# Kernel tuning notes

Measured on AMD Instinct MI355X. Metric: run time of the kernel, lower is better.

## Reference

```python
import jax, jax.numpy as jnp
import numpy as np

B, N, D, O, H, R = 32, 1024, 1024, 1024, 512, 64
TOPK = 4
MAX_GAIN = 0.1
SCALE = 1.0
LN_EPS = 1e-5


def _dct_basis(dim, num_bases):
    pos = np.arange(dim, dtype=np.float64)[None, :]
    modes = np.arange(num_bases, dtype=np.float64)[:, None]
    basis = np.cos(np.pi / dim * (pos + 0.5) * modes)
    basis[0] = basis[0] / np.sqrt(2.0)
    basis = basis * np.sqrt(2.0 / dim)
    return jnp.asarray(basis, jnp.float32)


def setup_inputs() -> dict:
    key = jax.random.key(0)
    ks = jax.random.split(key, 16)
    s = 0.02
    return {
        'x': jax.random.normal(ks[0], (B, N, D), jnp.float32),
        'context': jax.random.normal(ks[1], (B, H), jnp.float32),
        'input_basis': _dct_basis(D, R),                       # [R, D] (buffer)
        'output_basis': s * jax.random.normal(ks[2], (R, O), jnp.float32),
        'ln_gamma': jnp.ones((D,), jnp.float32),
        'ln_beta': jnp.zeros((D,), jnp.float32),
        'w1': s * jax.random.normal(ks[3], (D, H), jnp.float32),
        'b1': jnp.zeros((H,), jnp.float32),
        'w2': s * jax.random.normal(ks[4], (H, H), jnp.float32),
        'b2': jnp.zeros((H,), jnp.float32),
        'wg': s * jax.random.normal(ks[5], (H, R * R), jnp.float32),
        'bg': jnp.zeros((R * R,), jnp.float32),
        'wl': s * jax.random.normal(ks[6], (H, R * R), jnp.float32),
        'bl': jnp.zeros((R * R,), jnp.float32),
        'wm': s * jax.random.normal(ks[7], (2 * H, R), jnp.float32),
        'bm': 1.5 * jnp.ones((R,), jnp.float32),
        'wgain': s * jax.random.normal(ks[8], (2 * H, R), jnp.float32),
        'bgain': jnp.zeros((R,), jnp.float32),
        'wgate': s * jax.random.normal(ks[9], (2 * H, 1), jnp.float32),
        'bgate': -1.0 * jnp.ones((1,), jnp.float32),
        'wa': s * jax.random.normal(ks[10], (2 * H, 1), jnp.float32),
        'ba': -1.0 * jnp.ones((1,), jnp.float32),
        'wb': s * jax.random.normal(ks[11], (2 * H, 1), jnp.float32),
        'bb': jnp.zeros((1,), jnp.float32),
    }


def _detail_summary(x, topk):
    # x: [B, N, D] with token 0 = CLS; pick topk highest-variance patch tokens
    pt = x[:, 1:]                                   # [B, N-1, D]
    pm = jnp.mean(pt, axis=1, keepdims=True)
    scores = jnp.mean((pt - pm) ** 2, axis=-1)      # [B, N-1]
    _, idx = jax.lax.top_k(scores, topk)            # [B, k]
    gathered = jnp.take_along_axis(pt, idx[:, :, None], axis=1)  # [B, k, D]
    return jnp.mean(gathered, axis=1)               # [B, D]


def _skew(a):
    return 0.5 * (a - jnp.swapaxes(a, -1, -2))


def reference(x, context, input_basis, output_basis, ln_gamma, ln_beta,
              w1, b1, w2, b2, wg, bg, wl, bl, wm, bm,
              wgain, bgain, wgate, bgate, wa, ba, wb, bb):
    b = x.shape[0]
    r = input_basis.shape[0]

    detail = _detail_summary(x, TOPK)               # [B, D]
    mu = jnp.mean(detail, axis=-1, keepdims=True)
    var = jnp.var(detail, axis=-1, keepdims=True)
    h = (detail - mu) * jax.lax.rsqrt(var + LN_EPS) * ln_gamma + ln_beta
    h = jax.nn.gelu(h @ w1 + b1, approximate=False)
    local_context = h @ w2 + b2                     # [B, H]
    fused = jnp.concatenate([context, local_context], axis=-1)  # [B, 2H]

    global_skew = _skew((context @ wg + bg).reshape(b, r, r))
    local_skew = _skew((local_context @ wl + bl).reshape(b, r, r))
    mode_mask = jax.nn.sigmoid(fused @ wm + bm)     # [B, R]
    # diag(m) @ A @ diag(m) == m_i * A_ij * m_j
    mg = mode_mask[:, :, None] * global_skew * mode_mask[:, None, :]
    ml = mode_mask[:, :, None] * local_skew * mode_mask[:, None, :]
    comm = ml @ mg - mg @ ml                        # [B, R, R]

    alpha = SCALE * 0.5 * jax.nn.sigmoid(fused @ wa + ba)   # [B, 1]
    beta = SCALE * 0.25 * jnp.tanh(fused @ wb + bb)         # [B, 1]
    omega = alpha[:, :, None] * 0.5 * (mg + ml) + beta[:, :, None] * (comm / 12.0)

    q = jax.vmap(jax.scipy.linalg.expm)(omega)              # [B, R, R]
    gains = 1.0 + MAX_GAIN * jnp.tanh(fused @ wgain + bgain)  # [B, R]
    operator = q * gains[:, None, :]                        # q @ diag(gains)

    proj = jnp.einsum('bnd,rd->bnr', x, input_basis)        # [B, N, R]
    gate = SCALE * jax.nn.sigmoid(fused @ wgate + bgate)    # [B, 1]
    transformed = jnp.einsum('bnr,brk->bnk', proj, operator)
    delta = gate[:, None, :] * (transformed - proj)         # [B, N, R]
    out = jnp.einsum('bnr,ro->bno', delta, output_basis)    # [B, N, O]
    return out
```

## Files before the change

kernel.cpp:

```cpp
#include <hip/hip_runtime.h>
#include <math.h>

#define NB 32
#define NN 1024
#define ND 1024
#define NO 1024
#define NH 512
#define NR 64

#define OFF_PM     0u
#define OFF_PMSQ   32768u
#define OFF_ROWSQ  32800u
#define OFF_G      65568u
#define OFF_H0     98336u
#define OFF_H1     131104u
#define OFF_LOCAL  147488u
#define OFF_P1     163872u
#define OFF_P2     294944u
#define OFF_PG     360480u
#define OFF_PL     884768u
#define OFF_AG     1409056u
#define OFF_AL     1540128u
#define OFF_MASK   1671200u
#define OFF_GAINS  1673248u
#define OFF_SCAL   1675296u
#define OFF_MFIN   1675424u
#define OFF_C      1806496u
#define OFF_PROJ   3903648u
#define OFF_BT     6000800u

__global__ __launch_bounds__(256) void kT_basis(const float* __restrict__ basis, float* __restrict__ basisT){
  __shared__ float s[64][65];
  int d0 = blockIdx.x*64;
  int tid = threadIdx.x;
  #pragma unroll
  for(int i=0;i<16;i++){
    int idx = i*256 + tid;
    int r = idx>>6, dl = idx&63;
    s[r][dl] = basis[(size_t)r*ND + d0 + dl];
  }
  __syncthreads();
  #pragma unroll
  for(int i=0;i<16;i++){
    int idx = i*256 + tid;
    int dl = idx>>6, r = idx&63;
    basisT[(size_t)(d0+dl)*64 + r] = s[r][dl];
  }
}

__global__ __launch_bounds__(256) void k0_colsum(const float* __restrict__ x, float* __restrict__ part,
    float* __restrict__ rowsq){
  __shared__ float red[4][64];
  int tid = threadIdx.x;
  int nseg = blockIdx.x, b = blockIdx.y;
  int d4 = tid*4;
  int lane = tid & 63, wv = tid >> 6;
  const float* xp = x + (size_t)b*NN*ND + d4;
  int nstart = nseg*64; if(nseg==0) nstart = 1;
  int nend = nseg*64 + 64;
  float sx=0.f, sy=0.f, sz=0.f, sw=0.f;
  #pragma unroll 4
  for(int n=nstart; n<nend; n++){
    float4 v = *(const float4*)&xp[(size_t)n*ND];
    sx+=v.x; sy+=v.y; sz+=v.z; sw+=v.w;
    float s = v.x*v.x + v.y*v.y + v.z*v.z + v.w*v.w;
    #pragma unroll
    for(int o=32;o>0;o>>=1) s += __shfl_down(s, o);
    if(lane==0) red[wv][n - nseg*64] = s;
  }
  *(float4*)&part[(size_t)(b*16+nseg)*1024 + d4] = make_float4(sx,sy,sz,sw);
  __syncthreads();
  if(tid < 64 && !(nseg==0 && tid==0)){
    rowsq[b*1024 + nseg*64 + tid] = red[0][tid]+red[1][tid]+red[2][tid]+red[3][tid];
  }
}

__global__ __launch_bounds__(256) void k1_pmreduce(const float* __restrict__ part, float* __restrict__ pm, float* __restrict__ pmsq){
  __shared__ float red[256];
  int b = blockIdx.x, tid = threadIdx.x;
  float acc = 0.f;
  #pragma unroll
  for(int i=0;i<4;i++){
    int d = i*256 + tid;
    float s = 0.f;
    #pragma unroll
    for(int ks=0;ks<16;ks++) s += part[(size_t)(b*16+ks)*1024 + d];
    float p = s * (1.0f/1023.0f);
    pm[b*1024+d] = p;
    acc += p*p;
  }
  red[tid] = acc; __syncthreads();
  for(int o=128;o>0;o>>=1){ if(tid<o) red[tid]+=red[tid+o]; __syncthreads(); }
  if(tid==0) pmsq[b] = red[0]*(1.0f/1024.0f);
}

__global__ __launch_bounds__(256) void k2_proj(const float* __restrict__ x, const float* __restrict__ bT,
    const float* __restrict__ pm, float* __restrict__ proj, float* __restrict__ projp,
    float* __restrict__ G, float* __restrict__ Gp){
  __shared__ __align__(16) float xs[64][68];
  __shared__ __align__(16) float bs[64][68];
  int tid = threadIdx.x;
  int row0 = blockIdx.x*64;
  int b = row0 >> 10;
  int kh = blockIdx.y;
  int kbase = kh*512;
  int lrow = tid>>4, lkv = tid&15;
  int rg = tid>>4, cg = tid&15;
  float acc[4][4];
  #pragma unroll
  for(int i_=0;i_<4;i_++){ acc[i_][0]=0.f; acc[i_][1]=0.f; acc[i_][2]=0.f; acc[i_][3]=0.f; }
  float gp[4]={0.f,0.f,0.f,0.f};
  int sw = ((lkv>>1)&3)<<2;
  for(int kc=0;kc<8;kc++){
    int k0 = kbase + kc*64;
    float4 p4 = *(const float4*)&pm[(size_t)b*ND + k0 + lkv*4];
    #pragma unroll
    for(int i=0;i<4;i++){
      int r = lrow + 16*i;
      float4 v = *(const float4*)&x[((size_t)(row0+r))*ND + k0 + lkv*4];
      int rs = r ^ sw;
      xs[lkv*4+0][rs]=v.x; xs[lkv*4+1][rs]=v.y; xs[lkv*4+2][rs]=v.z; xs[lkv*4+3][rs]=v.w;
      gp[i] += v.x*p4.x + v.y*p4.y + v.z*p4.z + v.w*p4.w;
    }
    #pragma unroll
    for(int i=0;i<4;i++){
      int idx = tid + 256*i;
      int kk = idx>>4, kv = idx&15;
      *(float4*)&bs[kk][kv*4] = *(const float4*)&bT[((size_t)(k0+kk))*64 + kv*4];
    }
    __syncthreads();
    #pragma unroll 8
    for(int kk=0;kk<64;kk++){
      float4 a = *(const float4*)&xs[kk][ (rg ^ ((kk>>3)&3)) << 2 ];
      float4 bb= *(const float4*)&bs[kk][cg*4];
      float ar[4]={a.x,a.y,a.z,a.w};
      float br[4]={bb.x,bb.y,bb.z,bb.w};
      #pragma unroll
      for(int i_=0;i_<4;i_++){
        #pragma unroll
        for(int j_=0;j_<4;j_++) acc[i_][j_] += ar[i_]*br[j_];
      }
    }
    __syncthreads();
  }
  float* dst = kh ? projp : proj;
  #pragma unroll
  for(int i_=0;i_<4;i_++){
    float4 v = make_float4(acc[i_][0],acc[i_][1],acc[i_][2],acc[i_][3]);
    *(float4*)&dst[((size_t)(row0 + rg*4 + i_))*NR + cg*4] = v;
  }
  #pragma unroll
  for(int i=0;i<4;i++){ int r = lrow+16*i; bs[r][lkv]=gp[i]; }
  __syncthreads();
  if(tid<64){
    float g=0.f;
    #pragma unroll
    for(int c=0;c<16;c++) g += bs[tid][c];
    if(kh) Gp[row0+tid] = g; else G[row0+tid] = g;
  }
}

__global__ __launch_bounds__(256) void k2_red(float* __restrict__ proj, const float* __restrict__ projp){
  int id = blockIdx.x*256 + threadIdx.x;
  float4 a = *(const float4*)&proj[(size_t)id*4];
  float4 p = *(const float4*)&projp[(size_t)id*4];
  a.x+=p.x; a.y+=p.y; a.z+=p.z; a.w+=p.w;
  *(float4*)&proj[(size_t)id*4] = a;
}

__global__ __launch_bounds__(256) void k3_detail(const float* __restrict__ x, const float* __restrict__ rowsq,
    const float* __restrict__ G, const float* __restrict__ Gp, const float* __restrict__ pmsq,
    const float* __restrict__ gamma_, const float* __restrict__ beta_, float* __restrict__ h0){
  __shared__ float sc[1024];
  __shared__ float rv[256];
  __shared__ int ri[256];
  __shared__ int topi[4];
  __shared__ float mred[256];
  int b = blockIdx.x, tid = threadIdx.x;
  float ps = pmsq[b];
  const float invD = 1.0f/1024.0f;
  for(int n=tid;n<1024;n+=256)
    sc[n] = (n==0) ? -INFINITY : (rowsq[b*1024+n] - 2.0f*(G[b*1024+n]+Gp[b*1024+n]))*invD + ps;
  __syncthreads();
  for(int t=0;t<4;t++){
    float bv = -INFINITY; int bi = 0x7fffffff;
    for(int n=tid;n<1024;n+=256){
      float v = sc[n];
      if(v>bv || (v==bv && n<bi)){ bv=v; bi=n; }
    }
    rv[tid]=bv; ri[tid]=bi;
    __syncthreads();
    for(int o=128;o>0;o>>=1){
      if(tid<o){
        float v=rv[tid+o]; int ii=ri[tid+o];
        if(v>rv[tid] || (v==rv[tid] && ii<ri[tid])){ rv[tid]=v; ri[tid]=ii; }
      }
      __syncthreads();
    }
    if(tid==0){ topi[t]=ri[0]; sc[ri[0]] = -INFINITY; }
    __syncthreads();
  }
  int i0=topi[0], i1=topi[1], i2=topi[2], i3=topi[3];
  float dv[4]; float dsum=0.f;
  #pragma unroll
  for(int jj=0;jj<4;jj++){
    int d = tid + jj*256;
    float v = 0.25f*(x[((size_t)(b*NN+i0))*ND+d] + x[((size_t)(b*NN+i1))*ND+d]
                   + x[((size_t)(b*NN+i2))*ND+d] + x[((size_t)(b*NN+i3))*ND+d]);
    dv[jj]=v; dsum+=v;
  }
  mred[tid]=dsum; __syncthreads();
  for(int o=128;o>0;o>>=1){ if(tid<o) mred[tid]+=mred[tid+o]; __syncthreads(); }
  float mu = mred[0]*invD;
  __syncthreads();
  float vs=0.f;
  #pragma unroll
  for(int jj=0;jj<4;jj++){ float t2=dv[jj]-mu; vs+=t2*t2; }
  mred[tid]=vs; __syncthreads();
  for(int o=128;o>0;o>>=1){ if(tid<o) mred[tid]+=mred[tid+o]; __syncthreads(); }
  float var = mred[0]*invD;
  float rstd = rsqrtf(var + 1e-5f);
  #pragma unroll
  for(int jj=0;jj<4;jj++){
    int d = tid + jj*256;
    h0[b*1024+d] = (dv[jj]-mu)*rstd*gamma_[d] + beta_[d];
  }
}

__global__ __launch_bounds__(256) void gemm32_partial(const float* __restrict__ V, const float* __restrict__ W,
      float* __restrict__ part, int Kd, int Ncols){
  __shared__ __align__(16) float Vs[128][36];
  int col = blockIdx.x*256 + threadIdx.x;
  int k0 = blockIdx.y*128;
  for(int i=threadIdx.x; i<4096; i+=256){ int r=i>>7, k=i&127; Vs[k][r] = V[(size_t)r*Kd + k0 + k]; }
  __syncthreads();
  float acc[32];
  #pragma unroll
  for(int r=0;r<32;r++) acc[r]=0.f;
  #pragma unroll 4
  for(int k=0;k<128;k++){
    float wv = W[(size_t)(k0+k)*Ncols + col];
    #pragma unroll
    for(int r4=0;r4<8;r4++){
      float4 v = *(const float4*)&Vs[k][r4*4];
      acc[r4*4+0]+=v.x*wv; acc[r4*4+1]+=v.y*wv; acc[r4*4+2]+=v.z*wv; acc[r4*4+3]+=v.w*wv;
    }
  }
  #pragma unroll
  for(int r=0;r<32;r++) part[((size_t)(blockIdx.y*32 + r))*Ncols + col] = acc[r];
}

__global__ __launch_bounds__(256) void k_red_gelu(const float* __restrict__ part, const float* __restrict__ b1, float* __restrict__ h1){
  int id = blockIdx.x*256 + threadIdx.x;
  int b_ = id >> 9, j = id & 511;
  float s = b1[j];
  #pragma unroll
  for(int ks=0;ks<8;ks++) s += part[(size_t)(ks*32+b_)*512 + j];
  h1[id] = 0.5f*s*(1.0f + erff(s*0.70710678118654752440f));
}
__global__ __launch_bounds__(256) void k_red_local(const float* __restrict__ part, const float* __restrict__ b2, float* __restrict__ lcl){
  int id = blockIdx.x*256 + threadIdx.x;
  int b_ = id >> 9, j = id & 511;
  float s = b2[j];
  #pragma unroll
  for(int ks=0;ks<4;ks++) s += part[(size_t)(ks*32+b_)*512 + j];
  lcl[id] = s;
}
__global__ __launch_bounds__(256) void k_red_gl(const float* __restrict__ pg, const float* __restrict__ pl,
    const float* __restrict__ bg, const float* __restrict__ bl, float* __restrict__ Ag, float* __restrict__ Al){
  int id = blockIdx.x*256 + threadIdx.x;
  int c = id & 4095;
  int b_ = id >> 12;
  float sg = bg[c], sl = bl[c];
  #pragma unroll
  for(int ks=0;ks<4;ks++){
    sg += pg[(size_t)(ks*32 + b_)*4096 + c];
    sl += pl[(size_t)(ks*32 + b_)*4096 + c];
  }
  Ag[id] = sg; Al[id] = sl;
}

__global__ __launch_bounds__(1024) void k_heads(const float* __restrict__ context, const float* __restrict__ lcl,
    const float* __restrict__ wm, const float* __restrict__ bm,
    const float* __restrict__ wgain, const float* __restrict__ bgain,
    const float* __restrict__ wgate, const float* __restrict__ bgate,
    const float* __restrict__ wa, const float* __restrict__ ba,
    const float* __restrict__ wb, const float* __restrict__ bb,
    float* __restrict__ mask, float* __restrict__ gains, float* __restrict__ scal){
  __shared__ float fs[1024];
  __shared__ float redm[16][64];
  __shared__ float redg[16][64];
  __shared__ float wra[16], wrb[16], wrg[16];
  int b = blockIdx.x, tid = threadIdx.x;
  fs[tid] = (tid < 512) ? context[b*512 + tid] : lcl[b*512 + tid - 512];
  __syncthreads();
  int j = tid & 63, kq = tid >> 6;
  const float* wmp = wm    + (size_t)(kq*64)*64 + j;
  const float* wgp = wgain + (size_t)(kq*64)*64 + j;
  float am = 0.f, ag = 0.f;
  #pragma unroll 8
  for(int k=0;k<64;k++){
    float f = fs[kq*64 + k];
    am += f * wmp[k*64];
    ag += f * wgp[k*64];
  }
  redm[kq][j] = am; redg[kq][j] = ag;
  float f = fs[tid];
  float pa = f*wa[tid], pb = f*wb[tid], pg = f*wgate[tid];
  #pragma unroll
  for(int o=32;o>0;o>>=1){
    pa += __shfl_down(pa, o);
    pb += __shfl_down(pb, o);
    pg += __shfl_down(pg, o);
  }
  if(j == 0){ wra[kq]=pa; wrb[kq]=pb; wrg[kq]=pg; }
  __syncthreads();
  for(int o=8;o>0;o>>=1){
    if(kq < o){ redm[kq][j] += redm[kq+o][j]; redg[kq][j] += redg[kq+o][j]; }
    __syncthreads();
  }
  if(tid < 64){
    float m = redm[0][tid] + bm[tid];
    mask[b*64+tid] = 1.0f/(1.0f+expf(-m));
    float g = redg[0][tid] + bgain[tid];
    gains[b*64+tid] = 1.0f + 0.1f*tanhf(g);
  }
  if(tid == 0){
    float sa=0.f, sb=0.f, sg=0.f;
    #pragma unroll
    for(int i=0;i<16;i++){ sa+=wra[i]; sb+=wrb[i]; sg+=wrg[i]; }
    scal[b*4+0] = 0.5f/(1.0f+expf(-(sa+ba[0])));
    scal[b*4+1] = 0.25f*tanhf(sb+bb[0]);
    scal[b*4+2] = 1.0f/(1.0f+expf(-(sg+bgate[0])));
  }
}

__global__ __launch_bounds__(1024) void k7_expm(const float* __restrict__ Ag, const float* __restrict__ Al,
    const float* __restrict__ mask, const float* __restrict__ gains, const float* __restrict__ scal,
    float* __restrict__ Mfin){
  __shared__ __align__(16) float B0s[64][66];
  __shared__ __align__(16) float B1s[64][66];
  __shared__ __align__(16) float B2s[64][66];
  __shared__ float msks[64];
  __shared__ float colsum[64];
  __shared__ int ssh;
  int b = blockIdx.x, tid = threadIdx.x;
  int ig = tid>>5, jg = tid&31;
  int i0 = ig*2, j0 = jg*2;
  if(tid<64) msks[tid] = mask[b*64+tid];
  __syncthreads();
  float alpha = scal[b*4+0], bta = scal[b*4+1], gate = scal[b*4+2];
  const float* ag = Ag + b*4096;
  const float* al = Al + b*4096;
  #pragma unroll
  for(int di=0;di<2;di++){
    #pragma unroll
    for(int dj=0;dj<2;dj++){
      int i=i0+di, jx=j0+dj;
      float mm_ = msks[i]*msks[jx]*0.5f;
      B0s[i][jx] = mm_*(ag[i*64+jx]-ag[jx*64+i]);
      B1s[i][jx] = mm_*(al[i*64+jx]-al[jx*64+i]);
    }
  }
  __syncthreads();
  {
    float c00=0.f,c01=0.f,c10=0.f,c11=0.f;
    #pragma unroll 4
    for(int k=0;k<64;k++){
      float a0=B1s[i0][k], a1=B1s[i0+1][k];
      float m0=B0s[i0][k], m1=B0s[i0+1][k];
      float2 u = *(const float2*)&B0s[k][j0];
      float2 w = *(const float2*)&B1s[k][j0];
      c00 += a0*u.x - m0*w.x;  c01 += a0*u.y - m0*w.y;
      c10 += a1*u.x - m1*w.x;  c11 += a1*u.y - m1*w.y;
    }
    B2s[i0][j0]=c00; B2s[i0][j0+1]=c01; B2s[i0+1][j0]=c10; B2s[i0+1][j0+1]=c11;
  }
  __syncthreads();
  const float bc = bta*(1.0f/12.0f);
  #pragma unroll
  for(int di=0;di<2;di++){
    #pragma unroll
    for(int dj=0;dj<2;dj++){
      int i=i0+di, jx=j0+dj;
      B0s[i][jx] = alpha*0.5f*(B0s[i][jx]+B1s[i][jx]) + bc*B2s[i][jx];
    }
  }
  __syncthreads();
  if(tid<64){
    float s=0.f;
    for(int i=0;i<64;i++) s += fabsf(B0s[i][tid]);
    colsum[tid]=s;
  }
  __syncthreads();
  if(tid==0){
    float m=0.f;
    for(int jx=0;jx<64;jx++) m = fmaxf(m, colsum[jx]);
    int s=0;
    while(m>0.5f && s<30){ m*=0.5f; s++; }
    ssh = s;
  }
  __syncthreads();
  int sh = ssh;
  float scl = ldexpf(1.0f, -sh);
  #pragma unroll
  for(int di=0;di<2;di++){
    #pragma unroll
    for(int dj=0;dj<2;dj++){ int i=i0+di,jx=j0+dj; B0s[i][jx]*=scl; }
  }
  __syncthreads();
  #pragma unroll
  for(int di=0;di<2;di++){
    #pragma unroll
    for(int dj=0;dj<2;dj++){
      int i=i0+di, jx=j0+dj;
      B1s[i][jx] = ((i==jx)?1.0f:0.0f) + B0s[i][jx]*0.125f;
    }
  }
  __syncthreads();
  for(int kk=7;kk>=1;kk--){
    float c00=0.f,c01=0.f,c10=0.f,c11=0.f;
    #pragma unroll 4
    for(int k=0;k<64;k++){
      float a0=B0s[i0][k], a1=B0s[i0+1][k];
      float2 u = *(const float2*)&B1s[k][j0];
      c00+=a0*u.x; c01+=a0*u.y; c10+=a1*u.x; c11+=a1*u.y;
    }
    B2s[i0][j0]=c00; B2s[i0][j0+1]=c01; B2s[i0+1][j0]=c10; B2s[i0+1][j0+1]=c11;
    __syncthreads();
    float inv = 1.0f/(float)kk;
    #pragma unroll
    for(int di=0;di<2;di++){
      #pragma unroll
      for(int dj=0;dj<2;dj++){
        int i=i0+di, jx=j0+dj;
        B1s[i][jx] = ((i==jx)?1.0f:0.0f) + B2s[i][jx]*inv;
      }
    }
    __syncthreads();
  }
  float (*Q)[66] = B1s; float (*T)[66] = B2s;
  for(int t=0;t<sh;t++){
    float c00=0.f,c01=0.f,c10=0.f,c11=0.f;
    #pragma unroll 4
    for(int k=0;k<64;k++){
      float a0=Q[i0][k], a1=Q[i0+1][k];
      float2 u = *(const float2*)&Q[k][j0];
      c00+=a0*u.x; c01+=a0*u.y; c10+=a1*u.x; c11+=a1*u.y;
    }
    T[i0][j0]=c00; T[i0][j0+1]=c01; T[i0+1][j0]=c10; T[i0+1][j0+1]=c11;
    __syncthreads();
    float (*tmp)[66]=Q; Q=T; T=tmp;
  }
  float g0 = gains[b*64+j0], g1 = gains[b*64+j0+1];
  float* mf = Mfin + b*4096;
  #pragma unroll
  for(int di=0;di<2;di++){
    int i=i0+di;
    float2 v;
    v.x = gate*(Q[i][j0]*g0   - ((i==j0)?1.0f:0.0f));
    v.y = gate*(Q[i][j0+1]*g1 - ((i==j0+1)?1.0f:0.0f));
    *(float2*)&mf[i*64+j0] = v;
  }
}

__global__ __launch_bounds__(256) void k8_cmat(const float* __restrict__ Mfin, const float* __restrict__ ob, float* __restrict__ C){
  __shared__ __align__(16) float MT[64][68];
  int b = blockIdx.y; int o0 = blockIdx.x*128;
  int tid = threadIdx.x;
  for(int idx=tid; idx<4096; idx+=256){ int i=idx>>6, k=idx&63; MT[k][i] = Mfin[b*4096+idx]; }
  __syncthreads();
  int cg = tid&31, rg = tid>>5;
  float acc[8][4];
  #pragma unroll
  for(int r=0;r<8;r++){ acc[r][0]=0.f; acc[r][1]=0.f; acc[r][2]=0.f; acc[r][3]=0.f; }
  for(int k=0;k<64;k++){
    float4 bv = *(const float4*)&ob[(size_t)k*NO + o0 + cg*4];
    float4 a0 = *(const float4*)&MT[k][rg*8];
    float4 a1 = *(const float4*)&MT[k][rg*8+4];
    float arr[8]={a0.x,a0.y,a0.z,a0.w,a1.x,a1.y,a1.z,a1.w};
    #pragma unroll
    for(int r=0;r<8;r++){
      acc[r][0]+=arr[r]*bv.x; acc[r][1]+=arr[r]*bv.y; acc[r][2]+=arr[r]*bv.z; acc[r][3]+=arr[r]*bv.w;
    }
  }
  #pragma unroll
  for(int r=0;r<8;r++){
    *(float4*)&C[((size_t)(b*64 + rg*8+r))*NO + o0 + cg*4] = make_float4(acc[r][0],acc[r][1],acc[r][2],acc[r][3]);
  }
}

__global__ __launch_bounds__(256) void k9_out(const float* __restrict__ proj, const float* __restrict__ C, float* __restrict__ out){
  __shared__ __align__(16) float PT[64][132];
  __shared__ __align__(16) float CS[64][68];
  int b = blockIdx.z; int row0 = blockIdx.y*128; int o0 = blockIdx.x*64;
  int tid = threadIdx.x;
  #pragma unroll
  for(int i=0;i<8;i++){
    int f = tid + 256*i; int r = f>>4; int kv = f&15;
    float4 v = *(const float4*)&proj[((size_t)(b*NN + row0 + r))*NR + kv*4];
    PT[kv*4+0][r]=v.x; PT[kv*4+1][r]=v.y; PT[kv*4+2][r]=v.z; PT[kv*4+3][r]=v.w;
  }
  #pragma unroll
  for(int i=0;i<4;i++){
    int f = tid + 256*i; int k = f>>4; int kv = f&15;
    *(float4*)&CS[k][kv*4] = *(const float4*)&C[((size_t)(b*NR + k))*NO + o0 + kv*4];
  }
  __syncthreads();
  int rg = tid>>4, cg = tid&15;
  float acc[8][4];
  #pragma unroll
  for(int r=0;r<8;r++){ acc[r][0]=0.f; acc[r][1]=0.f; acc[r][2]=0.f; acc[r][3]=0.f; }
  #pragma unroll 8
  for(int k=0;k<64;k++){
    float4 bv = *(const float4*)&CS[k][cg*4];
    float4 a0 = *(const float4*)&PT[k][rg*8];
    float4 a1 = *(const float4*)&PT[k][rg*8+4];
    float arr[8]={a0.x,a0.y,a0.z,a0.w,a1.x,a1.y,a1.z,a1.w};
    #pragma unroll
    for(int r=0;r<8;r++){
      acc[r][0]+=arr[r]*bv.x; acc[r][1]+=arr[r]*bv.y; acc[r][2]+=arr[r]*bv.z; acc[r][3]+=arr[r]*bv.w;
    }
  }
  #pragma unroll
  for(int r=0;r<8;r++){
    *(float4*)&out[((size_t)(b*NN + row0 + rg*8 + r))*NO + o0 + cg*4] =
        make_float4(acc[r][0],acc[r][1],acc[r][2],acc[r][3]);
  }
}

extern "C" void kernel_launch(void* const* d_in, const int* in_sizes, int n_in,
                              void* d_out, int out_size, void* d_ws, size_t ws_size,
                              hipStream_t stream) {
  (void)in_sizes; (void)n_in; (void)out_size; (void)ws_size;
  const float* x       = (const float*)d_in[0];
  const float* context = (const float*)d_in[1];
  const float* ibasis  = (const float*)d_in[2];
  const float* obasis  = (const float*)d_in[3];
  const float* lng     = (const float*)d_in[4];
  const float* lnb     = (const float*)d_in[5];
  const float* w1      = (const float*)d_in[6];
  const float* b1      = (const float*)d_in[7];
  const float* w2      = (const float*)d_in[8];
  const float* b2      = (const float*)d_in[9];
  const float* wg      = (const float*)d_in[10];
  const float* bg      = (const float*)d_in[11];
  const float* wl      = (const float*)d_in[12];
  const float* bl      = (const float*)d_in[13];
  const float* wm      = (const float*)d_in[14];
  const float* bm      = (const float*)d_in[15];
  const float* wgain   = (const float*)d_in[16];
  const float* bgain   = (const float*)d_in[17];
  const float* wgate   = (const float*)d_in[18];
  const float* bgate   = (const float*)d_in[19];
  const float* wa      = (const float*)d_in[20];
  const float* ba      = (const float*)d_in[21];
  const float* wb      = (const float*)d_in[22];
  const float* bb      = (const float*)d_in[23];
  float* out = (float*)d_out;
  float* ws  = (float*)d_ws;

  float* pm    = ws + OFF_PM;
  float* pmsq  = ws + OFF_PMSQ;
  float* rowsq = ws + OFF_ROWSQ;
  float* G     = ws + OFF_G;
  float* h0    = ws + OFF_H0;
  float* h1    = ws + OFF_H1;
  float* lcl   = ws + OFF_LOCAL;
  float* p1    = ws + OFF_P1;
  float* p2    = ws + OFF_P2;
  float* pg_   = ws + OFF_PG;
  float* part  = ws + OFF_PG;
  float* Gp    = ws + OFF_PG;
  float* pl_   = ws + OFF_PL;
  float* Ag    = ws + OFF_AG;
  float* Al    = ws + OFF_AL;
  float* mask  = ws + OFF_MASK;
  float* gains = ws + OFF_GAINS;
  float* scal  = ws + OFF_SCAL;
  float* Mfin  = ws + OFF_MFIN;
  float* Cb    = ws + OFF_C;
  float* projp = ws + OFF_C;
  float* proj  = ws + OFF_PROJ;
  float* bT    = ws + OFF_BT;

  kT_basis<<<16,256,0,stream>>>(ibasis, bT);
  k0_colsum<<<dim3(16,NB),256,0,stream>>>(x, part, rowsq);
  k1_pmreduce<<<NB,256,0,stream>>>(part, pm, pmsq);
  k2_proj<<<dim3(512,2),256,0,stream>>>(x, bT, pm, proj, projp, G, Gp);
  k2_red<<<2048,256,0,stream>>>(proj, projp);
  k3_detail<<<NB,256,0,stream>>>(x, rowsq, G, Gp, pmsq, lng, lnb, h0);
  gemm32_partial<<<dim3(2,8),256,0,stream>>>(h0, w1, p1, 1024, 512);
  k_red_gelu<<<64,256,0,stream>>>(p1, b1, h1);
  gemm32_partial<<<dim3(2,4),256,0,stream>>>(h1, w2, p2, 512, 512);
  k_red_local<<<64,256,0,stream>>>(p2, b2, lcl);
  gemm32_partial<<<dim3(16,4),256,0,stream>>>(context, wg, pg_, 512, 4096);
  gemm32_partial<<<dim3(16,4),256,0,stream>>>(lcl, wl, pl_, 512, 4096);
  k_red_gl<<<512,256,0,stream>>>(pg_, pl_, bg, bl, Ag, Al);
  k_heads<<<NB,1024,0,stream>>>(context, lcl, wm, bm, wgain, bgain, wgate, bgate, wa, ba, wb, bb, mask, gains, scal);
  k7_expm<<<NB,1024,0,stream>>>(Ag, Al, mask, gains, scal, Mfin);
  k8_cmat<<<dim3(8,NB),256,0,stream>>>(Mfin, obasis, Cb);
  k9_out<<<dim3(16,8,NB),256,0,stream>>>(proj, Cb, out);
}
```

Before: 612.2 us.

## Fuse gl reduction, heads and expm into one kernel; batch wg/wl GEMMs

Merges the two context-to-generator GEMMs into one launch using a z-dimension, and folds the partial-sum reduction, head projections and the matrix exponential into a single per-batch kernel. Mask, gains and scalars stay in shared memory, so several global round-trips and launches go away. The expm matmuls are restructured so each thread computes a 1x4 output strip, with its A row held in registers as float4s. The shared padding changes to 68, and a missing sync in the projection kernel is added. The trade-off is higher register pressure from the 16-float4 row cache and the 1024-thread fused kernel.

```diff
diff --git a/kernel.cpp b/kernel.cpp
--- a/kernel.cpp
+++ b/kernel.cpp
@@ -19,15 +19,12 @@
 #define OFF_P2     294944u
 #define OFF_PG     360480u
 #define OFF_PL     884768u
-#define OFF_AG     1409056u
-#define OFF_AL     1540128u
-#define OFF_MASK   1671200u
-#define OFF_GAINS  1673248u
-#define OFF_SCAL   1675296u
 #define OFF_MFIN   1675424u
 #define OFF_C      1806496u
 #define OFF_PROJ   3903648u
 #define OFF_BT     6000800u
+
+#define AK(av,k) ((k&3)==0?av[(k)>>2].x:((k&3)==1?av[(k)>>2].y:((k&3)==2?av[(k)>>2].z:av[(k)>>2].w)))
 
 __global__ __launch_bounds__(256) void kT_basis(const float* __restrict__ basis, float* __restrict__ basisT){
   __shared__ float s[64][65];
@@ -149,6 +146,7 @@
     float4 v = make_float4(acc[i_][0],acc[i_][1],acc[i_][2],acc[i_][3]);
     *(float4*)&dst[((size_t)(row0 + rg*4 + i_))*NR + cg*4] = v;
   }
+  __syncthreads();
   #pragma unroll
   for(int i=0;i<4;i++){ int r = lrow+16*i; bs[r][lkv]=gp[i]; }
   __syncthreads();
@@ -250,6 +248,33 @@
   for(int r=0;r<32;r++) part[((size_t)(blockIdx.y*32 + r))*Ncols + col] = acc[r];
 }
 
+__global__ __launch_bounds__(256) void gemm32_gl(const float* __restrict__ ctx, const float* __restrict__ lcl,
+    const float* __restrict__ wg, const float* __restrict__ wl,
+    float* __restrict__ pg, float* __restrict__ pl){
+  __shared__ __align__(16) float Vs[128][36];
+  const float* V = blockIdx.z ? lcl : ctx;
+  const float* W = blockIdx.z ? wl : wg;
+  float* part    = blockIdx.z ? pl : pg;
+  int col = blockIdx.x*256 + threadIdx.x;
+  int k0 = blockIdx.y*128;
+  for(int i=threadIdx.x; i<4096; i+=256){ int r=i>>7, k=i&127; Vs[k][r] = V[(size_t)r*512 + k0 + k]; }
+  __syncthreads();
+  float acc[32];
+  #pragma unroll
+  for(int r=0;r<32;r++) acc[r]=0.f;
+  #pragma unroll 4
+  for(int k=0;k<128;k++){
+    float wv = W[(size_t)(k0+k)*4096 + col];
+    #pragma unroll
+    for(int r4=0;r4<8;r4++){
+      float4 v = *(const float4*)&Vs[k][r4*4];
+      acc[r4*4+0]+=v.x*wv; acc[r4*4+1]+=v.y*wv; acc[r4*4+2]+=v.z*wv; acc[r4*4+3]+=v.w*wv;
+    }
+  }
+  #pragma unroll
+  for(int r=0;r<32;r++) part[((size_t)(blockIdx.y*32 + r))*4096 + col] = acc[r];
+}
+
 __global__ __launch_bounds__(256) void k_red_gelu(const float* __restrict__ part, const float* __restrict__ b1, float* __restrict__ h1){
   int id = blockIdx.x*256 + threadIdx.x;
   int b_ = id >> 9, j = id & 511;
@@ -266,54 +291,70 @@
   for(int ks=0;ks<4;ks++) s += part[(size_t)(ks*32+b_)*512 + j];
   lcl[id] = s;
 }
-__global__ __launch_bounds__(256) void k_red_gl(const float* __restrict__ pg, const float* __restrict__ pl,
-    const float* __restrict__ bg, const float* __restrict__ bl, float* __restrict__ Ag, float* __restrict__ Al){
-  int id = blockIdx.x*256 + threadIdx.x;
-  int c = id & 4095;
-  int b_ = id >> 12;
-  float sg = bg[c], sl = bl[c];
-  #pragma unroll
-  for(int ks=0;ks<4;ks++){
-    sg += pg[(size_t)(ks*32 + b_)*4096 + c];
-    sl += pl[(size_t)(ks*32 + b_)*4096 + c];
-  }
-  Ag[id] = sg; Al[id] = sl;
-}
-
-__global__ __launch_bounds__(1024) void k_heads(const float* __restrict__ context, const float* __restrict__ lcl,
+
+__global__ __launch_bounds__(1024) void k7_fused(
+    const float* __restrict__ pg, const float* __restrict__ pl,
+    const float* __restrict__ bg, const float* __restrict__ bl,
+    const float* __restrict__ context, const float* __restrict__ lcl,
     const float* __restrict__ wm, const float* __restrict__ bm,
     const float* __restrict__ wgain, const float* __restrict__ bgain,
     const float* __restrict__ wgate, const float* __restrict__ bgate,
     const float* __restrict__ wa, const float* __restrict__ ba,
     const float* __restrict__ wb, const float* __restrict__ bb,
-    float* __restrict__ mask, float* __restrict__ gains, float* __restrict__ scal){
+    float* __restrict__ Mfin){
+  __shared__ __align__(16) float B0s[64][68];
+  __shared__ __align__(16) float B1s[64][68];
+  __shared__ __align__(16) float B2s[64][68];
   __shared__ float fs[1024];
   __shared__ float redm[16][64];
   __shared__ float redg[16][64];
   __shared__ float wra[16], wrb[16], wrg[16];
+  __shared__ float msks[64], gainss[64];
+  __shared__ float colsum[64];
+  __shared__ float sABG[3];
+  __shared__ int ssh;
   int b = blockIdx.x, tid = threadIdx.x;
+
+  int ig = tid>>5, jg = tid&31;
+  int i0 = ig*2, j0 = jg*2;
+  #pragma unroll
+  for(int di=0;di<2;di++){
+    #pragma unroll
+    for(int dj=0;dj<2;dj++){
+      int i=i0+di, jx=j0+dj, c=i*64+jx;
+      float sg = bg[c], sl = bl[c];
+      #pragma unroll
+      for(int ks=0;ks<4;ks++){
+        sg += pg[(size_t)(ks*32+b)*4096 + c];
+        sl += pl[(size_t)(ks*32+b)*4096 + c];
+      }
+      B0s[i][jx] = sg; B1s[i][jx] = sl;
+    }
+  }
   fs[tid] = (tid < 512) ? context[b*512 + tid] : lcl[b*512 + tid - 512];
   __syncthreads();
   int j = tid & 63, kq = tid >> 6;
-  const float* wmp = wm    + (size_t)(kq*64)*64 + j;
-  const float* wgp = wgain + (size_t)(kq*64)*64 + j;
-  float am = 0.f, ag = 0.f;
-  #pragma unroll 8
-  for(int k=0;k<64;k++){
-    float f = fs[kq*64 + k];
-    am += f * wmp[k*64];
-    ag += f * wgp[k*64];
-  }
-  redm[kq][j] = am; redg[kq][j] = ag;
-  float f = fs[tid];
-  float pa = f*wa[tid], pb = f*wb[tid], pg = f*wgate[tid];
-  #pragma unroll
-  for(int o=32;o>0;o>>=1){
-    pa += __shfl_down(pa, o);
-    pb += __shfl_down(pb, o);
-    pg += __shfl_down(pg, o);
-  }
-  if(j == 0){ wra[kq]=pa; wrb[kq]=pb; wrg[kq]=pg; }
+  {
+    const float* wmp = wm    + (size_t)(kq*64)*64 + j;
+    const float* wgp = wgain + (size_t)(kq*64)*64 + j;
+    float am = 0.f, ag = 0.f;
+    #pragma unroll 8
+    for(int k=0;k<64;k++){
+      float f = fs[kq*64 + k];
+      am += f * wmp[k*64];
+      ag += f * wgp[k*64];
+    }
+    redm[kq][j] = am; redg[kq][j] = ag;
+    float f = fs[tid];
+    float pa = f*wa[tid], pb = f*wb[tid], pgt = f*wgate[tid];
+    #pragma unroll
+    for(int o=32;o>0;o>>=1){
+      pa += __shfl_down(pa, o);
+      pb += __shfl_down(pb, o);
+      pgt += __shfl_down(pgt, o);
+    }
+    if(j == 0){ wra[kq]=pa; wrb[kq]=pb; wrg[kq]=pgt; }
+  }
   __syncthreads();
   for(int o=8;o>0;o>>=1){
     if(kq < o){ redm[kq][j] += redm[kq+o][j]; redg[kq][j] += redg[kq+o][j]; }
@@ -321,70 +362,81 @@
   }
   if(tid < 64){
     float m = redm[0][tid] + bm[tid];
-    mask[b*64+tid] = 1.0f/(1.0f+expf(-m));
+    msks[tid] = 1.0f/(1.0f+expf(-m));
     float g = redg[0][tid] + bgain[tid];
-    gains[b*64+tid] = 1.0f + 0.1f*tanhf(g);
+    gainss[tid] = 1.0f + 0.1f*tanhf(g);
   }
   if(tid == 0){
-    float sa=0.f, sb=0.f, sg=0.f;
-    #pragma unroll
-    for(int i=0;i<16;i++){ sa+=wra[i]; sb+=wrb[i]; sg+=wrg[i]; }
-    scal[b*4+0] = 0.5f/(1.0f+expf(-(sa+ba[0])));
-    scal[b*4+1] = 0.25f*tanhf(sb+bb[0]);
-    scal[b*4+2] = 1.0f/(1.0f+expf(-(sg+bgate[0])));
-  }
-}
-
-__global__ __launch_bounds__(1024) void k7_expm(const float* __restrict__ Ag, const float* __restrict__ Al,
-    const float* __restrict__ mask, const float* __restrict__ gains, const float* __restrict__ scal,
-    float* __restrict__ Mfin){
-  __shared__ __align__(16) float B0s[64][66];
-  __shared__ __align__(16) float B1s[64][66];
-  __shared__ __align__(16) float B2s[64][66];
-  __shared__ float msks[64];
-  __shared__ float colsum[64];
-  __shared__ int ssh;
-  int b = blockIdx.x, tid = threadIdx.x;
-  int ig = tid>>5, jg = tid&31;
-  int i0 = ig*2, j0 = jg*2;
-  if(tid<64) msks[tid] = mask[b*64+tid];
-  __syncthreads();
-  float alpha = scal[b*4+0], bta = scal[b*4+1], gate = scal[b*4+2];
-  const float* ag = Ag + b*4096;
-  const float* al = Al + b*4096;
+    float sa=0.f, sb=0.f, sg2=0.f;
+    #pragma unroll
+    for(int i=0;i<16;i++){ sa+=wra[i]; sb+=wrb[i]; sg2+=wrg[i]; }
+    sABG[0] = 0.5f/(1.0f+expf(-(sa+ba[0])));
+    sABG[1] = 0.25f*tanhf(sb+bb[0]);
+    sABG[2] = 1.0f/(1.0f+expf(-(sg2+bgate[0])));
+  }
+  __syncthreads();
+  float alpha = sABG[0], bta = sABG[1], gate = sABG[2];
+  float mgr[2][2], mlr[2][2];
   #pragma unroll
   for(int di=0;di<2;di++){
     #pragma unroll
     for(int dj=0;dj<2;dj++){
       int i=i0+di, jx=j0+dj;
       float mm_ = msks[i]*msks[jx]*0.5f;
-      B0s[i][jx] = mm_*(ag[i*64+jx]-ag[jx*64+i]);
-      B1s[i][jx] = mm_*(al[i*64+jx]-al[jx*64+i]);
-    }
-  }
-  __syncthreads();
-  {
-    float c00=0.f,c01=0.f,c10=0.f,c11=0.f;
-    #pragma unroll 4
-    for(int k=0;k<64;k++){
-      float a0=B1s[i0][k], a1=B1s[i0+1][k];
-      float m0=B0s[i0][k], m1=B0s[i0+1][k];
-      float2 u = *(const float2*)&B0s[k][j0];
-      float2 w = *(const float2*)&B1s[k][j0];
-      c00 += a0*u.x - m0*w.x;  c01 += a0*u.y - m0*w.y;
-      c10 += a1*u.x - m1*w.x;  c11 += a1*u.y - m1*w.y;
-    }
-    B2s[i0][j0]=c00; B2s[i0][j0+1]=c01; B2s[i0+1][j0]=c10; B2s[i0+1][j0+1]=c11;
-  }
-  __syncthreads();
-  const float bc = bta*(1.0f/12.0f);
+      mgr[di][dj] = mm_*(B0s[i][jx]-B0s[jx][i]);
+      mlr[di][dj] = mm_*(B1s[i][jx]-B1s[jx][i]);
+    }
+  }
+  __syncthreads();
   #pragma unroll
   for(int di=0;di<2;di++){
     #pragma unroll
     for(int dj=0;dj<2;dj++){
       int i=i0+di, jx=j0+dj;
-      B0s[i][jx] = alpha*0.5f*(B0s[i][jx]+B1s[i][jx]) + bc*B2s[i][jx];
-    }
+      B0s[i][jx] = mgr[di][dj];
+      B1s[i][jx] = mlr[di][dj];
+    }
+  }
+  __syncthreads();
+  int ir = tid>>4, cgc = tid&15;
+  int jc = cgc*4;
+  float4 av[16];
+  {
+    const float* rowp = &B1s[ir][0];
+    #pragma unroll
+    for(int q=0;q<16;q++) av[q] = *(const float4*)(rowp + q*4);
+    float4 t1 = make_float4(0.f,0.f,0.f,0.f);
+    #pragma unroll
+    for(int k=0;k<64;k++){
+      float4 bv = *(const float4*)&B0s[k][jc];
+      float a = AK(av,k);
+      t1.x += a*bv.x; t1.y += a*bv.y; t1.z += a*bv.z; t1.w += a*bv.w;
+    }
+    const float* rowq = &B0s[ir][0];
+    #pragma unroll
+    for(int q=0;q<16;q++) av[q] = *(const float4*)(rowq + q*4);
+    float4 t2 = make_float4(0.f,0.f,0.f,0.f);
+    #pragma unroll
+    for(int k=0;k<64;k++){
+      float4 bv = *(const float4*)&B1s[k][jc];
+      float a = AK(av,k);
+      t2.x += a*bv.x; t2.y += a*bv.y; t2.z += a*bv.z; t2.w += a*bv.w;
+    }
+    float4 cm = make_float4(t1.x-t2.x, t1.y-t2.y, t1.z-t2.z, t1.w-t2.w);
+    *(float4*)&B2s[ir][jc] = cm;
+  }
+  __syncthreads();
+  {
+    const float bc = bta*(1.0f/12.0f);
+    float4 g4 = *(const float4*)&B0s[ir][jc];
+    float4 l4 = *(const float4*)&B1s[ir][jc];
+    float4 c4 = *(const float4*)&B2s[ir][jc];
+    float4 o4;
+    o4.x = alpha*0.5f*(g4.x+l4.x) + bc*c4.x;
+    o4.y = alpha*0.5f*(g4.y+l4.y) + bc*c4.y;
+    o4.z = alpha*0.5f*(g4.z+l4.z) + bc*c4.z;
+    o4.w = alpha*0.5f*(g4.w+l4.w) + bc*c4.w;
+    *(float4*)&B0s[ir][jc] = o4;
   }
   __syncthreads();
   if(tid<64){
@@ -403,64 +455,66 @@
   __syncthreads();
   int sh = ssh;
   float scl = ldexpf(1.0f, -sh);
-  #pragma unroll
-  for(int di=0;di<2;di++){
-    #pragma unroll
-    for(int dj=0;dj<2;dj++){ int i=i0+di,jx=j0+dj; B0s[i][jx]*=scl; }
-  }
-  __syncthreads();
-  #pragma unroll
-  for(int di=0;di<2;di++){
-    #pragma unroll
-    for(int dj=0;dj<2;dj++){
-      int i=i0+di, jx=j0+dj;
-      B1s[i][jx] = ((i==jx)?1.0f:0.0f) + B0s[i][jx]*0.125f;
-    }
-  }
-  __syncthreads();
+  {
+    float4 a4 = *(const float4*)&B0s[ir][jc];
+    a4.x*=scl; a4.y*=scl; a4.z*=scl; a4.w*=scl;
+    *(float4*)&B0s[ir][jc] = a4;
+    float4 p4;
+    p4.x = ((ir==jc+0)?1.0f:0.0f) + a4.x*0.125f;
+    p4.y = ((ir==jc+1)?1.0f:0.0f) + a4.y*0.125f;
+    p4.z = ((ir==jc+2)?1.0f:0.0f) + a4.z*0.125f;
+    p4.w = ((ir==jc+3)?1.0f:0.0f) + a4.w*0.125f;
+    *(float4*)&B1s[ir][jc] = p4;
+  }
+  __syncthreads();
+  {
+    const float* rowp = &B0s[ir][0];
+    #pragma unroll
+    for(int q=0;q<16;q++) av[q] = *(const float4*)(rowp + q*4);
+  }
+  float* P = &B1s[0][0];
+  float* T = &B2s[0][0];
   for(int kk=7;kk>=1;kk--){
-    float c00=0.f,c01=0.f,c10=0.f,c11=0.f;
-    #pragma unroll 4
+    float4 acc = make_float4(0.f,0.f,0.f,0.f);
+    #pragma unroll
     for(int k=0;k<64;k++){
-      float a0=B0s[i0][k], a1=B0s[i0+1][k];
-      float2 u = *(const float2*)&B1s[k][j0];
-      c00+=a0*u.x; c01+=a0*u.y; c10+=a1*u.x; c11+=a1*u.y;
-    }
-    B2s[i0][j0]=c00; B2s[i0][j0+1]=c01; B2s[i0+1][j0]=c10; B2s[i0+1][j0+1]=c11;
+      float4 bv = *(const float4*)&P[(size_t)k*68 + jc];
+      float a = AK(av,k);
+      acc.x += a*bv.x; acc.y += a*bv.y; acc.z += a*bv.z; acc.w += a*bv.w;
+    }
+    float inv = 1.0f/(float)kk;
+    float4 o4;
+    o4.x = ((ir==jc+0)?1.0f:0.0f) + acc.x*inv;
+    o4.y = ((ir==jc+1)?1.0f:0.0f) + acc.y*inv;
+    o4.z = ((ir==jc+2)?1.0f:0.0f) + acc.z*inv;
+    o4.w = ((ir==jc+3)?1.0f:0.0f) + acc.w*inv;
+    *(float4*)&T[(size_t)ir*68 + jc] = o4;
     __syncthreads();
-    float inv = 1.0f/(float)kk;
-    #pragma unroll
-    for(int di=0;di<2;di++){
-      #pragma unroll
-      for(int dj=0;dj<2;dj++){
-        int i=i0+di, jx=j0+dj;
-        B1s[i][jx] = ((i==jx)?1.0f:0.0f) + B2s[i][jx]*inv;
-      }
-    }
+    float* tmp = P; P = T; T = tmp;
+  }
+  float* S = (P == &B1s[0][0]) ? &B2s[0][0] : &B1s[0][0];
+  for(int t=0;t<sh;t++){
+    #pragma unroll
+    for(int q=0;q<16;q++) av[q] = *(const float4*)(P + (size_t)ir*68 + q*4);
+    float4 acc = make_float4(0.f,0.f,0.f,0.f);
+    #pragma unroll
+    for(int k=0;k<64;k++){
+      float4 bv = *(const float4*)&P[(size_t)k*68 + jc];
+      float a = AK(av,k);
+      acc.x += a*bv.x; acc.y += a*bv.y; acc.z += a*bv.z; acc.w += a*bv.w;
+    }
+    *(float4*)&S[(size_t)ir*68 + jc] = acc;
     __syncthreads();
-  }
-  float (*Q)[66] = B1s; float (*T)[66] = B2s;
-  for(int t=0;t<sh;t++){
-    float c00=0.f,c01=0.f,c10=0.f,c11=0.f;
-    #pragma unroll 4
-    for(int k=0;k<64;k++){
-      float a0=Q[i0][k], a1=Q[i0+1][k];
-      float2 u = *(const float2*)&Q[k][j0];
-      c00+=a0*u.x; c01+=a0*u.y; c10+=a1*u.x; c11+=a1*u.y;
-    }
-    T[i0][j0]=c00; T[i0][j0+1]=c01; T[i0+1][j0]=c10; T[i0+1][j0+1]=c11;
-    __syncthreads();
-    float (*tmp)[66]=Q; Q=T; T=tmp;
-  }
-  float g0 = gains[b*64+j0], g1 = gains[b*64+j0+1];
-  float* mf = Mfin + b*4096;
-  #pragma unroll
-  for(int di=0;di<2;di++){
-    int i=i0+di;
-    float2 v;
-    v.x = gate*(Q[i][j0]*g0   - ((i==j0)?1.0f:0.0f));
-    v.y = gate*(Q[i][j0+1]*g1 - ((i==j0+1)?1.0f:0.0f));
-    *(float2*)&mf[i*64+j0] = v;
+    float* tmp = P; P = S; S = tmp;
+  }
+  {
+    float4 q4 = *(const float4*)&P[(size_t)ir*68 + jc];
+    float4 v;
+    v.x = gate*(q4.x*gainss[jc+0] - ((ir==jc+0)?1.0f:0.0f));
+    v.y = gate*(q4.y*gainss[jc+1] - ((ir==jc+1)?1.0f:0.0f));
+    v.z = gate*(q4.z*gainss[jc+2] - ((ir==jc+2)?1.0f:0.0f));
+    v.w = gate*(q4.w*gainss[jc+3] - ((ir==jc+3)?1.0f:0.0f));
+    *(float4*)&Mfin[(size_t)b*4096 + ir*64 + jc] = v;
   }
 }
 
@@ -573,11 +627,6 @@
   float* part  = ws + OFF_PG;
   float* Gp    = ws + OFF_PG;
   float* pl_   = ws + OFF_PL;
-  float* Ag    = ws + OFF_AG;
-  float* Al    = ws + OFF_AL;
-  float* mask  = ws + OFF_MASK;
-  float* gains = ws + OFF_GAINS;
-  float* scal  = ws + OFF_SCAL;
   float* Mfin  = ws + OFF_MFIN;
   float* Cb    = ws + OFF_C;
   float* projp = ws + OFF_C;
@@ -594,11 +643,9 @@
   k_red_gelu<<<64,256,0,stream>>>(p1, b1, h1);
   gemm32_partial<<<dim3(2,4),256,0,stream>>>(h1, w2, p2, 512, 512);
   k_red_local<<<64,256,0,stream>>>(p2, b2, lcl);
-  gemm32_partial<<<dim3(16,4),256,0,stream>>>(context, wg, pg_, 512, 4096);
-  gemm32_partial<<<dim3(16,4),256,0,stream>>>(lcl, wl, pl_, 512, 4096);
-  k_red_gl<<<512,256,0,stream>>>(pg_, pl_, bg, bl, Ag, Al);
-  k_heads<<<NB,1024,0,stream>>>(context, lcl, wm, bm, wgain, bgain, wgate, bgate, wa, ba, wb, bb, mask, gains, scal);
-  k7_expm<<<NB,1024,0,stream>>>(Ag, Al, mask, gains, scal, Mfin);
+  gemm32_gl<<<dim3(16,4,2),256,0,stream>>>(context, lcl, wg, wl, pg_, pl_);
+  k7_fused<<<NB,1024,0,stream>>>(pg_, pl_, bg, bl, context, lcl, wm, bm, wgain, bgain,
+                                 wgate, bgate, wa, ba, wb, bb, Mfin);
   k8_cmat<<<dim3(8,NB),256,0,stream>>>(Mfin, obasis, Cb);
   k9_out<<<dim3(16,8,NB),256,0,stream>>>(proj, Cb, out);
 }
```

After: 580.6 us. -5.2%, faster.
